# Kernel optimization log

Measured on AMD Instinct MI355X. Metric: run time of the kernel, lower is better.

Reference implementation:

```python
import jax, jax.numpy as jnp
import numpy as np
import itertools

BATCH = 8192
NUM_FIELDS = 30
VOCAB = 100000
DIM = 64
ATT_DIM = DIM // 2


def setup_inputs() -> dict:
    key = jax.random.key(0)
    ks = jax.random.split(key, 12)
    x = jax.random.randint(ks[0], (BATCH, NUM_FIELDS), 0, VOCAB)
    emb = jax.random.normal(ks[1], (VOCAB, DIM), dtype=jnp.float32) * 0.05
    W = jax.random.normal(ks[2], (DIM, ATT_DIM), dtype=jnp.float32) * (1.0 / np.sqrt(DIM))
    b = jnp.zeros((ATT_DIM,), dtype=jnp.float32)
    h = jax.random.normal(ks[3], (ATT_DIM,), dtype=jnp.float32) * 0.05
    d1_w = jax.random.normal(ks[4], (DIM // 2, DIM), dtype=jnp.float32) * (1.0 / np.sqrt(DIM))
    d1_b = jnp.zeros((DIM // 2,), dtype=jnp.float32)
    d2_w = jax.random.normal(ks[5], (DIM // 4, DIM // 2), dtype=jnp.float32) * (1.0 / np.sqrt(DIM // 2))
    d2_b = jnp.zeros((DIM // 4,), dtype=jnp.float32)
    ffn_w = jax.random.normal(ks[6], (1, DIM // 4), dtype=jnp.float32) * (1.0 / np.sqrt(DIM // 4))
    ffn_b = jnp.zeros((1,), dtype=jnp.float32)
    return {"x": x, "emb": emb, "W": W, "b": b, "h": h,
            "d1_w": d1_w, "d1_b": d1_b, "d2_w": d2_w, "d2_b": d2_b,
            "ffn_w": ffn_w, "ffn_b": ffn_b}


# static pairwise combination indices over the field axis
_ROW, _COL = map(np.asarray, zip(*itertools.combinations(range(NUM_FIELDS), 2)))


def reference(x, emb, W, b, h, d1_w, d1_b, d2_w, d2_b, ffn_w, ffn_b):
    e = emb[x]                                   # [B, F, D] embedding gather
    half_bip = e[:, _ROW] * e[:, _COL]           # [B, P, D] pairwise products, P=C(F,2)
    att_h = jax.nn.relu(jnp.einsum('bpd,da->bpa', half_bip, W) + b)  # [B, P, A]
    att = jax.nn.softmax(att_h @ h, axis=-1)     # [B, P]
    pooled = jnp.einsum('bpd,bp->bd', half_bip, att)  # attention-weighted sum -> [B, D]
    out = jax.nn.relu(pooled @ d1_w.T + d1_b)    # [B, D/2]
    out = jax.nn.relu(out @ d2_w.T + d2_b)       # [B, D/4]
    logits = jax.nn.sigmoid(out @ ffn_w.T + ffn_b)  # [B, 1]
    return logits
```

## Files before the change

kernel.cpp:

```cpp
#include <hip/hip_runtime.h>
#include <hip/hip_fp16.h>
#include <math.h>

#define NF   30
#define NP   435
#define NPAD 448
#define NT   14
#define DIM  64
#define ATT  32
#define WAS  40
#define BPB  4

typedef __attribute__((ext_vector_type(8)))  _Float16 half8v;
typedef __attribute__((ext_vector_type(16))) float    f32x16;

struct IJTab { unsigned short v[NPAD]; };
static constexpr IJTab make_ij() {
    IJTab t{};
    int p = 0;
    for (int i = 0; i < NF; ++i)
        for (int j = i + 1; j < NF; ++j)
            t.v[p++] = (unsigned short)(i | (j << 8));
    for (; p < NPAD; ++p) t.v[p] = (unsigned short)(31 | (31 << 8));
    return t;
}
__constant__ IJTab IJ = make_ij();

__device__ __forceinline__ int eh_off(int row, int d) {
    return (row << 6) + ((((d >> 3) ^ (row & 7)) << 3) | (d & 7));
}
__device__ __forceinline__ int ua_off(int i, int j) {
    return (i << 5) + ((((j >> 3) ^ (i & 7)) << 3) | (j & 7));
}

struct __align__(16) WaveCtx {
    _Float16 Eh[32 * 64];
    _Float16 UA[32 * 32];
    float    pooled[DIM];
    float    h1[32];
    float    h2[16];
};

__launch_bounds__(256, 5)
__global__ void afm_wave_kernel(const int*   __restrict__ x,
                                const float* __restrict__ emb,
                                const float* __restrict__ W,
                                const float* __restrict__ bb,
                                const float* __restrict__ hh,
                                const float* __restrict__ d1w,
                                const float* __restrict__ d1b,
                                const float* __restrict__ d2w,
                                const float* __restrict__ d2b,
                                const float* __restrict__ fw,
                                const float* __restrict__ fb,
                                float* __restrict__ out,
                                int Btot)
{
    __shared__ WaveCtx ctx[BPB];
    __shared__ __align__(16) _Float16 Wt[32][WAS];

    const int t    = threadIdx.x;
    const int lane = t & 63;
    const int w    = t >> 6;
    const int col  = lane & 31;
    const int half = lane >> 5;
    const int b    = blockIdx.x * BPB + w;

    WaveCtx& C = ctx[w];

    {
        const int a = t >> 3, kb = (t & 7) * 8;
        half8v w8;
        #pragma unroll
        for (int e = 0; e < 8; ++e) w8[e] = (_Float16)W[(kb + e) * ATT + a];
        *(half8v*)&Wt[a][kb] = w8;
    }
    if (b < Btot) {
        #pragma unroll
        for (int it = 0; it < 4; ++it) {
            const int s = it * 64 + lane;
            const int row = s >> 3, blk = s & 7;
            half8v v8 = {};
            if (row < NF) {
                const int xr = x[b * NF + row];
                const float4 f0 = *(const float4*)&emb[(long)xr * DIM + blk * 8];
                const float4 f1 = *(const float4*)&emb[(long)xr * DIM + blk * 8 + 4];
                v8[0] = (_Float16)f0.x; v8[1] = (_Float16)f0.y;
                v8[2] = (_Float16)f0.z; v8[3] = (_Float16)f0.w;
                v8[4] = (_Float16)f1.x; v8[5] = (_Float16)f1.y;
                v8[6] = (_Float16)f1.z; v8[7] = (_Float16)f1.w;
            }
            *(half8v*)&C.Eh[(row << 6) + ((blk ^ (row & 7)) << 3)] = v8;
        }
        const float4 z = make_float4(0.f, 0.f, 0.f, 0.f);
        ((float4*)C.UA)[lane]      = z;
        ((float4*)C.UA)[lane + 64] = z;
    }
    __syncthreads();

    if (b >= Btot) return;

    half8v wfrag[4];
    #pragma unroll
    for (int ks = 0; ks < 4; ++ks)
        wfrag[ks] = *(const half8v*)&Wt[col][ks * 16 + half * 8];

    float4 b4[4], h4[4];
    #pragma unroll
    for (int q = 0; q < 4; ++q) {
        b4[q] = *(const float4*)&bb[8 * q + 4 * half];
        h4[q] = *(const float4*)&hh[8 * q + 4 * half];
    }

    float wsum = 0.f;
    #pragma unroll 2
    for (int tile = 0; tile < NT; ++tile) {
        const int p  = tile * 32 + col;
        const int pj = IJ.v[p];
        const int fi = pj & 255, fj = pj >> 8;
        const _Float16* Ei = &C.Eh[fi << 6];
        const _Float16* Ej = &C.Eh[fj << 6];
        const int si = fi & 7, sj = fj & 7;
        f32x16 acc = {};
        #pragma unroll
        for (int ks = 0; ks < 4; ++ks) {
            const int blk = 2 * ks + half;
            const half8v va = *(const half8v*)&Ei[(blk ^ si) << 3];
            const half8v vc = *(const half8v*)&Ej[(blk ^ sj) << 3];
            const half8v bp = va * vc;
            acc = __builtin_amdgcn_mfma_f32_32x32x16_f16(wfrag[ks], bp, acc, 0, 0, 0);
        }
        float sv = 0.f;
        #pragma unroll
        for (int q = 0; q < 4; ++q) {
            sv += fmaxf(acc[4 * q + 0] + b4[q].x, 0.f) * h4[q].x;
            sv += fmaxf(acc[4 * q + 1] + b4[q].y, 0.f) * h4[q].y;
            sv += fmaxf(acc[4 * q + 2] + b4[q].z, 0.f) * h4[q].z;
            sv += fmaxf(acc[4 * q + 3] + b4[q].w, 0.f) * h4[q].w;
        }
        sv += __shfl_xor(sv, 32);
        if (half == 0 && p < NP) {
            const float ex = __expf(sv);
            C.UA[ua_off(fi, fj)] = (_Float16)ex;
            wsum += ex;
        }
    }
    #pragma unroll
    for (int o = 1; o <= 16; o <<= 1) wsum += __shfl_xor(wsum, o);
    const float inv_sum = 1.f / wsum;

    half8v uaf[2];
    #pragma unroll
    for (int ks = 0; ks < 2; ++ks)
        uaf[ks] = *(const half8v*)&C.UA[(col << 5) + (((2 * ks + half) ^ (col & 7)) << 3)];
    #pragma unroll
    for (int dh = 0; dh < 2; ++dh) {
        const int d = col + 32 * dh;
        f32x16 tacc = {};
        #pragma unroll
        for (int ks = 0; ks < 2; ++ks) {
            const int j0 = ks * 16 + half * 8;
            half8v eb;
            #pragma unroll
            for (int e = 0; e < 8; ++e) eb[e] = C.Eh[eh_off(j0 + e, d)];
            tacc = __builtin_amdgcn_mfma_f32_32x32x16_f16(uaf[ks], eb, tacc, 0, 0, 0);
        }
        float sv = 0.f;
        #pragma unroll
        for (int q = 0; q < 4; ++q) {
            const int i0 = 8 * q + 4 * half;
            #pragma unroll
            for (int s = 0; s < 4; ++s)
                sv += (float)C.Eh[eh_off(i0 + s, d)] * tacc[4 * q + s];
        }
        sv += __shfl_xor(sv, 32);
        if (half == 0) C.pooled[d] = sv * inv_sum;
    }

    {
        const int o = lane >> 1, part = lane & 1;
        const float* wr = &d1w[o * DIM + part * 32];
        const float* pp = &C.pooled[part * 32];
        float a1 = 0.f;
        #pragma unroll
        for (int k = 0; k < 32; ++k) a1 = fmaf(pp[k], wr[k], a1);
        a1 += __shfl_xor(a1, 1);
        if (part == 0) C.h1[o] = fmaxf(a1 + d1b[o], 0.f);
    }
    {
        const int o = lane >> 2, part = lane & 3;
        float a2 = 0.f;
        #pragma unroll
        for (int k = 0; k < 8; ++k)
            a2 = fmaf(C.h1[part * 8 + k], d2w[o * 32 + part * 8 + k], a2);
        a2 += __shfl_xor(a2, 1);
        a2 += __shfl_xor(a2, 2);
        if (part == 0) C.h2[o] = fmaxf(a2 + d2b[o], 0.f);
    }
    if (lane < 16) {
        float v = C.h2[lane] * fw[lane];
        #pragma unroll
        for (int o2 = 1; o2 < 16; o2 <<= 1) v += __shfl_xor(v, o2);
        if (lane == 0) out[b] = 1.f / (1.f + __expf(-(v + fb[0])));
    }
}

extern "C" void kernel_launch(void* const* d_in, const int* in_sizes, int n_in,
                              void* d_out, int out_size, void* d_ws, size_t ws_size,
                              hipStream_t stream) {
    (void)n_in; (void)d_ws; (void)ws_size; (void)out_size;
    const int*   x   = (const int*)  d_in[0];
    const float* emb = (const float*)d_in[1];
    const float* W   = (const float*)d_in[2];
    const float* bbp = (const float*)d_in[3];
    const float* hhp = (const float*)d_in[4];
    const float* d1w = (const float*)d_in[5];
    const float* d1b = (const float*)d_in[6];
    const float* d2w = (const float*)d_in[7];
    const float* d2b = (const float*)d_in[8];
    const float* fw  = (const float*)d_in[9];
    const float* fb  = (const float*)d_in[10];
    float* out = (float*)d_out;

    const int B = in_sizes[0] / NF;
    const int grid = (B + BPB - 1) / BPB;
    afm_wave_kernel<<<grid, 256, 0, stream>>>(x, emb, W, bbp, hhp,
                                              d1w, d1b, d2w, d2b, fw, fb, out, B);
}
```

Measured before the change: 44.83 us.

## Reorganize LDS embedding layout to block-major, union UA with MLP scratch

Stores the fp16 embeddings in LDS as [block][row][8] instead of an XOR-swizzled row-major layout, which removes the swizzle address arithmetic in the pair and pooling loops. The attention-score buffer is overlaid with the MLP scratch through a union to cut per-wave LDS use, and launch bounds are raised to allow 6 blocks per CU. The bias is folded into the MFMA accumulator's initial value, the tile loop unroll is reduced to 1, and the d1 dot product is vectorized with float4 loads. The risks are more LDS bank conflicts from the unswizzled layout and less instruction-level parallelism in the tile loop.

```diff
diff --git a/kernel.cpp b/kernel.cpp
--- a/kernel.cpp
+++ b/kernel.cpp
@@ -26,22 +26,15 @@
 }
 __constant__ IJTab IJ = make_ij();
 
-__device__ __forceinline__ int eh_off(int row, int d) {
-    return (row << 6) + ((((d >> 3) ^ (row & 7)) << 3) | (d & 7));
-}
-__device__ __forceinline__ int ua_off(int i, int j) {
-    return (i << 5) + ((((j >> 3) ^ (i & 7)) << 3) | (j & 7));
-}
-
 struct __align__(16) WaveCtx {
-    _Float16 Eh[32 * 64];
-    _Float16 UA[32 * 32];
-    float    pooled[DIM];
-    float    h1[32];
-    float    h2[16];
+    _Float16 Eh[8][32][8];
+    union {
+        _Float16 UA[4][32][8];
+        struct { float pooled[DIM]; float h1[32]; float h2[16]; } mlp;
+    };
 };
 
-__launch_bounds__(256, 5)
+__launch_bounds__(256, 6)
 __global__ void afm_wave_kernel(const int*   __restrict__ x,
                                 const float* __restrict__ emb,
                                 const float* __restrict__ W,
@@ -90,7 +83,7 @@
                 v8[4] = (_Float16)f1.x; v8[5] = (_Float16)f1.y;
                 v8[6] = (_Float16)f1.z; v8[7] = (_Float16)f1.w;
             }
-            *(half8v*)&C.Eh[(row << 6) + ((blk ^ (row & 7)) << 3)] = v8;
+            *(half8v*)&C.Eh[blk][row][0] = v8;
         }
         const float4 z = make_float4(0.f, 0.f, 0.f, 0.f);
         ((float4*)C.UA)[lane]      = z;
@@ -112,36 +105,40 @@
         h4[q] = *(const float4*)&hh[8 * q + 4 * half];
     }
 
+    const _Float16* EhB = &C.Eh[0][0][0] + (half << 8);
+
     float wsum = 0.f;
-    #pragma unroll 2
+    #pragma unroll 1
     for (int tile = 0; tile < NT; ++tile) {
         const int p  = tile * 32 + col;
         const int pj = IJ.v[p];
         const int fi = pj & 255, fj = pj >> 8;
-        const _Float16* Ei = &C.Eh[fi << 6];
-        const _Float16* Ej = &C.Eh[fj << 6];
-        const int si = fi & 7, sj = fj & 7;
-        f32x16 acc = {};
+        const _Float16* Ei = EhB + (fi << 3);
+        const _Float16* Ej = EhB + (fj << 3);
+        f32x16 acc;
+        #pragma unroll
+        for (int q = 0; q < 4; ++q) {
+            acc[4 * q + 0] = b4[q].x; acc[4 * q + 1] = b4[q].y;
+            acc[4 * q + 2] = b4[q].z; acc[4 * q + 3] = b4[q].w;
+        }
         #pragma unroll
         for (int ks = 0; ks < 4; ++ks) {
-            const int blk = 2 * ks + half;
-            const half8v va = *(const half8v*)&Ei[(blk ^ si) << 3];
-            const half8v vc = *(const half8v*)&Ej[(blk ^ sj) << 3];
-            const half8v bp = va * vc;
-            acc = __builtin_amdgcn_mfma_f32_32x32x16_f16(wfrag[ks], bp, acc, 0, 0, 0);
+            const half8v va = *(const half8v*)(Ei + ks * 512);
+            const half8v vc = *(const half8v*)(Ej + ks * 512);
+            acc = __builtin_amdgcn_mfma_f32_32x32x16_f16(wfrag[ks], va * vc, acc, 0, 0, 0);
         }
         float sv = 0.f;
         #pragma unroll
         for (int q = 0; q < 4; ++q) {
-            sv += fmaxf(acc[4 * q + 0] + b4[q].x, 0.f) * h4[q].x;
-            sv += fmaxf(acc[4 * q + 1] + b4[q].y, 0.f) * h4[q].y;
-            sv += fmaxf(acc[4 * q + 2] + b4[q].z, 0.f) * h4[q].z;
-            sv += fmaxf(acc[4 * q + 3] + b4[q].w, 0.f) * h4[q].w;
+            sv += fmaxf(acc[4 * q + 0], 0.f) * h4[q].x;
+            sv += fmaxf(acc[4 * q + 1], 0.f) * h4[q].y;
+            sv += fmaxf(acc[4 * q + 2], 0.f) * h4[q].z;
+            sv += fmaxf(acc[4 * q + 3], 0.f) * h4[q].w;
         }
         sv += __shfl_xor(sv, 32);
         if (half == 0 && p < NP) {
             const float ex = __expf(sv);
-            C.UA[ua_off(fi, fj)] = (_Float16)ex;
+            C.UA[fj >> 3][fi][fj & 7] = (_Float16)ex;
             wsum += ex;
         }
     }
@@ -149,56 +146,62 @@
     for (int o = 1; o <= 16; o <<= 1) wsum += __shfl_xor(wsum, o);
     const float inv_sum = 1.f / wsum;
 
-    half8v uaf[2];
-    #pragma unroll
-    for (int ks = 0; ks < 2; ++ks)
-        uaf[ks] = *(const half8v*)&C.UA[(col << 5) + (((2 * ks + half) ^ (col & 7)) << 3)];
+    const _Float16* UAb = (const _Float16*)C.UA + (half << 8) + (col << 3);
+    const half8v uaf0 = *(const half8v*)(UAb);
+    const half8v uaf1 = *(const half8v*)(UAb + 512);
     #pragma unroll
     for (int dh = 0; dh < 2; ++dh) {
         const int d = col + 32 * dh;
+        const _Float16* Bd  = &C.Eh[0][0][0] + ((d >> 3) << 8) + (d & 7);
+        const _Float16* BdB = Bd + (half << 6);
         f32x16 tacc = {};
         #pragma unroll
         for (int ks = 0; ks < 2; ++ks) {
-            const int j0 = ks * 16 + half * 8;
             half8v eb;
             #pragma unroll
-            for (int e = 0; e < 8; ++e) eb[e] = C.Eh[eh_off(j0 + e, d)];
-            tacc = __builtin_amdgcn_mfma_f32_32x32x16_f16(uaf[ks], eb, tacc, 0, 0, 0);
-        }
+            for (int e = 0; e < 8; ++e) eb[e] = BdB[ks * 128 + e * 8];
+            tacc = __builtin_amdgcn_mfma_f32_32x32x16_f16(ks ? uaf1 : uaf0, eb, tacc, 0, 0, 0);
+        }
+        const _Float16* BdC = Bd + (half << 5);
         float sv = 0.f;
         #pragma unroll
         for (int q = 0; q < 4; ++q) {
-            const int i0 = 8 * q + 4 * half;
             #pragma unroll
             for (int s = 0; s < 4; ++s)
-                sv += (float)C.Eh[eh_off(i0 + s, d)] * tacc[4 * q + s];
+                sv += (float)BdC[(q << 6) + (s << 3)] * tacc[4 * q + s];
         }
         sv += __shfl_xor(sv, 32);
-        if (half == 0) C.pooled[d] = sv * inv_sum;
+        if (half == 0) C.mlp.pooled[d] = sv * inv_sum;
     }
 
     {
         const int o = lane >> 1, part = lane & 1;
-        const float* wr = &d1w[o * DIM + part * 32];
-        const float* pp = &C.pooled[part * 32];
+        const float4* wr4 = (const float4*)&d1w[o * DIM + part * 32];
+        const float4* pp4 = (const float4*)&C.mlp.pooled[part * 32];
         float a1 = 0.f;
         #pragma unroll
-        for (int k = 0; k < 32; ++k) a1 = fmaf(pp[k], wr[k], a1);
+        for (int k = 0; k < 8; ++k) {
+            const float4 wv = wr4[k], pv = pp4[k];
+            a1 = fmaf(pv.x, wv.x, a1);
+            a1 = fmaf(pv.y, wv.y, a1);
+            a1 = fmaf(pv.z, wv.z, a1);
+            a1 = fmaf(pv.w, wv.w, a1);
+        }
         a1 += __shfl_xor(a1, 1);
-        if (part == 0) C.h1[o] = fmaxf(a1 + d1b[o], 0.f);
+        if (part == 0) C.mlp.h1[o] = fmaxf(a1 + d1b[o], 0.f);
     }
     {
         const int o = lane >> 2, part = lane & 3;
         float a2 = 0.f;
         #pragma unroll
         for (int k = 0; k < 8; ++k)
-            a2 = fmaf(C.h1[part * 8 + k], d2w[o * 32 + part * 8 + k], a2);
+            a2 = fmaf(C.mlp.h1[part * 8 + k], d2w[o * 32 + part * 8 + k], a2);
         a2 += __shfl_xor(a2, 1);
         a2 += __shfl_xor(a2, 2);
-        if (part == 0) C.h2[o] = fmaxf(a2 + d2b[o], 0.f);
+        if (part == 0) C.mlp.h2[o] = fmaxf(a2 + d2b[o], 0.f);
     }
     if (lane < 16) {
-        float v = C.h2[lane] * fw[lane];
+        float v = C.mlp.h2[lane] * fw[lane];
         #pragma unroll
         for (int o2 = 1; o2 < 16; o2 <<= 1) v += __shfl_xor(v, o2);
         if (lane == 0) out[b] = 1.f / (1.f + __expf(-(v + fb[0])));
```

New measurement: 66.40 us. 1.48x slower.

## Split each batch row across two waves with block-level reduction

Applied to the files above, without the earlier changes.

Each batch row is now handled by a pair of waves instead of one. The waves share the embedding gather, split the 14 pair tiles between them, and each computes half of the pooled output dimensions. The softmax denominator is combined through shared memory, which adds extra __syncthreads. Rows per block drop from 4 to 2, and the occupancy hint goes from 5 to 4 blocks. The aim is shorter per-row latency and more waves working on the MFMA stage, at the cost of more barriers and an MLP tail where half the waves sit idle.

```diff
diff --git a/kernel.cpp b/kernel.cpp
--- a/kernel.cpp
+++ b/kernel.cpp
@@ -9,7 +9,7 @@
 #define DIM  64
 #define ATT  32
 #define WAS  40
-#define BPB  4
+#define BPB  2
 
 typedef __attribute__((ext_vector_type(8)))  _Float16 half8v;
 typedef __attribute__((ext_vector_type(16))) float    f32x16;
@@ -29,19 +29,17 @@
 __device__ __forceinline__ int eh_off(int row, int d) {
     return (row << 6) + ((((d >> 3) ^ (row & 7)) << 3) | (d & 7));
 }
-__device__ __forceinline__ int ua_off(int i, int j) {
-    return (i << 5) + ((((j >> 3) ^ (i & 7)) << 3) | (j & 7));
-}
 
 struct __align__(16) WaveCtx {
     _Float16 Eh[32 * 64];
     _Float16 UA[32 * 32];
     float    pooled[DIM];
+    float    red[2];
     float    h1[32];
     float    h2[16];
 };
 
-__launch_bounds__(256, 5)
+__launch_bounds__(256, 4)
 __global__ void afm_wave_kernel(const int*   __restrict__ x,
                                 const float* __restrict__ emb,
                                 const float* __restrict__ W,
@@ -61,12 +59,15 @@
 
     const int t    = threadIdx.x;
     const int lane = t & 63;
-    const int w    = t >> 6;
+    const int wv   = t >> 6;
+    const int pr   = wv >> 1;
+    const int h    = wv & 1;
     const int col  = lane & 31;
     const int half = lane >> 5;
-    const int b    = blockIdx.x * BPB + w;
-
-    WaveCtx& C = ctx[w];
+    const int b    = blockIdx.x * BPB + pr;
+    const int bc   = (b < Btot) ? b : (Btot - 1);
+
+    WaveCtx& C = ctx[pr];
 
     {
         const int a = t >> 3, kb = (t & 7) * 8;
@@ -75,30 +76,27 @@
         for (int e = 0; e < 8; ++e) w8[e] = (_Float16)W[(kb + e) * ATT + a];
         *(half8v*)&Wt[a][kb] = w8;
     }
-    if (b < Btot) {
-        #pragma unroll
-        for (int it = 0; it < 4; ++it) {
-            const int s = it * 64 + lane;
-            const int row = s >> 3, blk = s & 7;
-            half8v v8 = {};
-            if (row < NF) {
-                const int xr = x[b * NF + row];
-                const float4 f0 = *(const float4*)&emb[(long)xr * DIM + blk * 8];
-                const float4 f1 = *(const float4*)&emb[(long)xr * DIM + blk * 8 + 4];
-                v8[0] = (_Float16)f0.x; v8[1] = (_Float16)f0.y;
-                v8[2] = (_Float16)f0.z; v8[3] = (_Float16)f0.w;
-                v8[4] = (_Float16)f1.x; v8[5] = (_Float16)f1.y;
-                v8[6] = (_Float16)f1.z; v8[7] = (_Float16)f1.w;
-            }
-            *(half8v*)&C.Eh[(row << 6) + ((blk ^ (row & 7)) << 3)] = v8;
-        }
+    #pragma unroll
+    for (int it = 0; it < 2; ++it) {
+        const int s = h * 128 + it * 64 + lane;
+        const int row = s >> 3, blk = s & 7;
+        half8v v8 = {};
+        if (row < NF) {
+            const int xr = x[bc * NF + row];
+            const float4 f0 = *(const float4*)&emb[(long)xr * DIM + blk * 8];
+            const float4 f1 = *(const float4*)&emb[(long)xr * DIM + blk * 8 + 4];
+            v8[0] = (_Float16)f0.x; v8[1] = (_Float16)f0.y;
+            v8[2] = (_Float16)f0.z; v8[3] = (_Float16)f0.w;
+            v8[4] = (_Float16)f1.x; v8[5] = (_Float16)f1.y;
+            v8[6] = (_Float16)f1.z; v8[7] = (_Float16)f1.w;
+        }
+        *(half8v*)&C.Eh[(row << 6) + ((blk ^ (row & 7)) << 3)] = v8;
+    }
+    {
         const float4 z = make_float4(0.f, 0.f, 0.f, 0.f);
-        ((float4*)C.UA)[lane]      = z;
-        ((float4*)C.UA)[lane + 64] = z;
+        ((float4*)C.UA)[h * 64 + lane] = z;
     }
     __syncthreads();
-
-    if (b >= Btot) return;
 
     half8v wfrag[4];
     #pragma unroll
@@ -113,8 +111,9 @@
     }
 
     float wsum = 0.f;
-    #pragma unroll 2
-    for (int tile = 0; tile < NT; ++tile) {
+    #pragma unroll 1
+    for (int tt = 0; tt < 7; ++tt) {
+        const int tile = 2 * tt + h;
         const int p  = tile * 32 + col;
         const int pj = IJ.v[p];
         const int fi = pj & 255, fj = pj >> 8;
@@ -127,8 +126,7 @@
             const int blk = 2 * ks + half;
             const half8v va = *(const half8v*)&Ei[(blk ^ si) << 3];
             const half8v vc = *(const half8v*)&Ej[(blk ^ sj) << 3];
-            const half8v bp = va * vc;
-            acc = __builtin_amdgcn_mfma_f32_32x32x16_f16(wfrag[ks], bp, acc, 0, 0, 0);
+            acc = __builtin_amdgcn_mfma_f32_32x32x16_f16(wfrag[ks], va * vc, acc, 0, 0, 0);
         }
         float sv = 0.f;
         #pragma unroll
@@ -141,21 +139,22 @@
         sv += __shfl_xor(sv, 32);
         if (half == 0 && p < NP) {
             const float ex = __expf(sv);
-            C.UA[ua_off(fi, fj)] = (_Float16)ex;
+            C.UA[(fi << 5) + ((((fj >> 3) ^ (fi & 7)) << 3) | (fj & 7))] = (_Float16)ex;
             wsum += ex;
         }
     }
     #pragma unroll
     for (int o = 1; o <= 16; o <<= 1) wsum += __shfl_xor(wsum, o);
-    const float inv_sum = 1.f / wsum;
-
-    half8v uaf[2];
-    #pragma unroll
-    for (int ks = 0; ks < 2; ++ks)
-        uaf[ks] = *(const half8v*)&C.UA[(col << 5) + (((2 * ks + half) ^ (col & 7)) << 3)];
-    #pragma unroll
-    for (int dh = 0; dh < 2; ++dh) {
-        const int d = col + 32 * dh;
+    if (lane == 0) C.red[h] = wsum;
+    __syncthreads();
+    const float inv_sum = 1.f / (C.red[0] + C.red[1]);
+
+    {
+        const int d = col + 32 * h;
+        half8v uaf[2];
+        #pragma unroll
+        for (int ks = 0; ks < 2; ++ks)
+            uaf[ks] = *(const half8v*)&C.UA[(col << 5) + (((2 * ks + half) ^ (col & 7)) << 3)];
         f32x16 tacc = {};
         #pragma unroll
         for (int ks = 0; ks < 2; ++ks) {
@@ -176,32 +175,42 @@
         sv += __shfl_xor(sv, 32);
         if (half == 0) C.pooled[d] = sv * inv_sum;
     }
-
-    {
-        const int o = lane >> 1, part = lane & 1;
-        const float* wr = &d1w[o * DIM + part * 32];
-        const float* pp = &C.pooled[part * 32];
-        float a1 = 0.f;
-        #pragma unroll
-        for (int k = 0; k < 32; ++k) a1 = fmaf(pp[k], wr[k], a1);
-        a1 += __shfl_xor(a1, 1);
-        if (part == 0) C.h1[o] = fmaxf(a1 + d1b[o], 0.f);
-    }
-    {
-        const int o = lane >> 2, part = lane & 3;
-        float a2 = 0.f;
-        #pragma unroll
-        for (int k = 0; k < 8; ++k)
-            a2 = fmaf(C.h1[part * 8 + k], d2w[o * 32 + part * 8 + k], a2);
-        a2 += __shfl_xor(a2, 1);
-        a2 += __shfl_xor(a2, 2);
-        if (part == 0) C.h2[o] = fmaxf(a2 + d2b[o], 0.f);
-    }
-    if (lane < 16) {
-        float v = C.h2[lane] * fw[lane];
-        #pragma unroll
-        for (int o2 = 1; o2 < 16; o2 <<= 1) v += __shfl_xor(v, o2);
-        if (lane == 0) out[b] = 1.f / (1.f + __expf(-(v + fb[0])));
+    __syncthreads();
+
+    if (h == 0) {
+        {
+            const int o = lane >> 1, part = lane & 1;
+            const float4* wr4 = (const float4*)&d1w[o * DIM + part * 32];
+            const float4* pp4 = (const float4*)&C.pooled[part * 32];
+            float a1 = 0.f;
+            #pragma unroll
+            for (int k = 0; k < 8; ++k) {
+                const float4 wvv = wr4[k], pv = pp4[k];
+                a1 = fmaf(pv.x, wvv.x, a1);
+                a1 = fmaf(pv.y, wvv.y, a1);
+                a1 = fmaf(pv.z, wvv.z, a1);
+                a1 = fmaf(pv.w, wvv.w, a1);
+            }
+            a1 += __shfl_xor(a1, 1);
+            if (part == 0) C.h1[o] = fmaxf(a1 + d1b[o], 0.f);
+        }
+        {
+            const int o = lane >> 2, part = lane & 3;
+            float a2 = 0.f;
+            #pragma unroll
+            for (int k = 0; k < 8; ++k)
+                a2 = fmaf(C.h1[part * 8 + k], d2w[o * 32 + part * 8 + k], a2);
+            a2 += __shfl_xor(a2, 1);
+            a2 += __shfl_xor(a2, 2);
+            if (part == 0) C.h2[o] = fmaxf(a2 + d2b[o], 0.f);
+        }
+        if (lane < 16) {
+            float v = C.h2[lane] * fw[lane];
+            #pragma unroll
+            for (int o2 = 1; o2 < 16; o2 <<= 1) v += __shfl_xor(v, o2);
+            if (lane == 0 && b < Btot)
+                out[b] = 1.f / (1.f + __expf(-(v + fb[0])));
+        }
     }
 }
 
```

New measurement: 50.52 us. 1.13x slower.
